# Kernel optimization log

Measured on AMD Instinct MI355X. Metric: run time of the kernel, lower is better.

The kernel has to match this reference:

```python
import jax, jax.numpy as jnp
import numpy as np

B, S, HID, H = 2, 2048, 1024, 16
D_HEAD = HID // H  # 64
EPS = 1e-5


def _gammas():
    lo, hi = np.log(1.0 / 512.0), np.log(1.0 / 32.0)
    return (1.0 - np.exp(np.linspace(lo, hi, H))).astype(np.float32)


def _decay_mask():
    # D[h, n, m] = gamma_h^(n-m) for n >= m else 0  (causal exponential decay)
    gam = jnp.asarray(_gammas())                      # [H]
    pos = jnp.arange(S, dtype=jnp.float32)
    diff = pos[:, None] - pos[None, :]                # [S, S]
    keep = diff >= 0
    logg = jnp.log(gam)[:, None, None]                # [H,1,1]
    safe = jnp.where(keep, diff, 0.0)[None]           # avoid inf for masked entries
    return jnp.where(keep[None], jnp.exp(safe * logg), 0.0)  # [H, S, S]


def setup_inputs() -> dict:
    key = jax.random.key(0)
    ks = jax.random.split(key, 10)
    rn = lambda k, shape, s=1.0: jax.random.normal(k, shape, dtype=jnp.float32) * s
    return {
        "x": rn(ks[0], (B, S, HID)),
        "wq": rn(ks[1], (H, D_HEAD, D_HEAD), 1.0 / np.sqrt(D_HEAD)),
        "bq": rn(ks[2], (H, D_HEAD), 0.02),
        "wk": rn(ks[3], (H, D_HEAD, D_HEAD), 1.0 / np.sqrt(D_HEAD)),
        "bk": rn(ks[4], (H, D_HEAD), 0.02),
        "wv": rn(ks[5], (H, D_HEAD, D_HEAD), 1.0 / np.sqrt(D_HEAD)),
        "theta": rn(ks[6], (H, D_HEAD), 1.0 / D_HEAD),
        "gn_weight": jnp.ones((HID,), jnp.float32),
        "gn_bias": jnp.zeros((HID,), jnp.float32),
        "weight1": rn(ks[7], (HID, HID), 1.0 / HID),
        "weight2": rn(ks[8], (HID, HID), 1.0 / HID),
    }


def reference(x, wq, bq, wk, bk, wv, theta, gn_weight, gn_bias, weight1, weight2):
    # Per-head retention (all heads vectorized; torch loops over heads).
    xh = x.reshape(B, S, H, D_HEAD)
    q = jnp.einsum('bshd,hde->bshe', xh, wq) + bq
    k = jnp.einsum('bshd,hde->bshe', xh, wk) + bk
    v = jnp.einsum('bshd,hde->bshe', xh, wv)
    # Complex rotary factors exp(i*n*theta) on q, conj on k -> real part of q k^H:
    ang = jnp.arange(S, dtype=jnp.float32)[:, None, None] * theta[None]  # [S,H,d]
    cs, sn = jnp.cos(ang), jnp.sin(ang)
    scores = (jnp.einsum('bshd,bthd->bhst', q * cs, k * cs)
              + jnp.einsum('bshd,bthd->bhst', q * sn, k * sn))  # Re(QK^H) [B,H,S,S]
    scores = scores * _decay_mask()[None]                        # decay mask
    ret = jnp.einsum('bhst,bthd->bshd', scores, v)               # [B,S,H,d]
    # GroupNorm with groups = n_heads over channels (per-head normalization).
    mean = jnp.mean(ret, axis=-1, keepdims=True)
    var = jnp.var(ret, axis=-1, keepdims=True)
    retn = (ret - mean) * jax.lax.rsqrt(var + EPS)
    retn = retn.reshape(B, S, HID) * gn_weight + gn_bias
    # Swish gate on x @ W1, residual add, project with W2.
    gate = x @ weight1
    out = gate * jax.nn.sigmoid(gate) + retn
    return out @ weight2
```

## Files before the change

### kernel.cpp

```cpp
#include <hip/hip_runtime.h>
#include <cstdint>
#include <cstddef>

#define B_ 2
#define S_ 2048
#define HID_ 1024
#define H_ 16
#define DH_ 64

typedef __attribute__((ext_vector_type(8))) short short8;
typedef __attribute__((ext_vector_type(8))) unsigned short ushort8;
typedef __attribute__((ext_vector_type(4))) unsigned short ushort4v;
typedef __attribute__((ext_vector_type(4))) float floatx4;
typedef __attribute__((ext_vector_type(4))) float float4v;

static __device__ __forceinline__ unsigned short f2bf(float f) {
  unsigned int u = __float_as_uint(f);
  u += 0x7fffu + ((u >> 16) & 1u);
  return (unsigned short)(u >> 16);
}
static __device__ __forceinline__ float bf2f(unsigned short h) {
  return __uint_as_float(((unsigned int)h) << 16);
}

__global__ __launch_bounds__(256) void convert_kernel(
    const float* __restrict__ x, const float* __restrict__ w1,
    const float* __restrict__ w2, unsigned short* __restrict__ x_bf,
    unsigned short* __restrict__ w1t, unsigned short* __restrict__ w2t_hi,
    unsigned short* __restrict__ w2t_lo) {
  const int NX = B_ * S_ * HID_;
  const int NW = HID_ * HID_;
  int idx = blockIdx.x * 256 + threadIdx.x;
  if (idx < NX) {
    x_bf[idx] = f2bf(x[idx]);
  } else if (idx < NX + NW) {
    int i = idx - NX;
    int n = i >> 10, k = i & 1023;
    w1t[i] = f2bf(w1[k * HID_ + n]);
  } else if (idx < NX + 2 * NW) {
    int i = idx - NX - NW;
    int n = i >> 10, k = i & 1023;
    float v = w2[k * HID_ + n];
    unsigned short h = f2bf(v);
    w2t_hi[i] = h;
    w2t_lo[i] = f2bf(v - bf2f(h));
  }
}

__global__ __launch_bounds__(256) void qkv_kernel(
    const float* __restrict__ x, const float* __restrict__ wq,
    const float* __restrict__ bq, const float* __restrict__ wk,
    const float* __restrict__ bk, const float* __restrict__ wv,
    const float* __restrict__ theta,
    unsigned short* __restrict__ q_h, unsigned short* __restrict__ q_l,
    unsigned short* __restrict__ k_h, unsigned short* __restrict__ k_l,
    unsigned short* __restrict__ v_th, unsigned short* __restrict__ v_tl,
    int b) {
  __shared__ __align__(16) float xs[64 * 68];
  __shared__ __align__(16) float wqs[64 * 68];
  __shared__ __align__(16) float wks[64 * 68];
  __shared__ __align__(16) float wvs[64 * 68];

  int tid = threadIdx.x;
  int st = blockIdx.x, h = blockIdx.y;
  int s0 = st * 64;

#pragma unroll
  for (int i = 0; i < 4; ++i) {
    int cid = tid + i * 256;
    int r = cid >> 4, c4 = (cid & 15) * 4;
    *reinterpret_cast<float4v*>(&xs[r * 68 + c4]) =
        *reinterpret_cast<const float4v*>(x + ((size_t)(b * S_ + s0 + r)) * HID_ + h * DH_ + c4);
  }
#pragma unroll
  for (int i = 0; i < 4; ++i) {
    int cid = tid + i * 256;
    int d = cid >> 4, c4 = (cid & 15) * 4;
    *reinterpret_cast<float4v*>(&wqs[d * 68 + c4]) =
        *reinterpret_cast<const float4v*>(wq + (size_t)(h * DH_ + d) * DH_ + c4);
    *reinterpret_cast<float4v*>(&wks[d * 68 + c4]) =
        *reinterpret_cast<const float4v*>(wk + (size_t)(h * DH_ + d) * DH_ + c4);
    *reinterpret_cast<float4v*>(&wvs[d * 68 + c4]) =
        *reinterpret_cast<const float4v*>(wv + (size_t)(h * DH_ + d) * DH_ + c4);
  }
  __syncthreads();

  int rg = tid >> 3;
  int cg = tid & 7;
  int r0 = rg * 2, c0 = cg * 8;

  float aq[2][8], ak[2][8], av[2][8];
#pragma unroll
  for (int i = 0; i < 2; ++i)
#pragma unroll
    for (int j = 0; j < 8; ++j) { aq[i][j] = 0.f; ak[i][j] = 0.f; av[i][j] = 0.f; }

  for (int d = 0; d < 64; ++d) {
    float x0 = xs[(r0 + 0) * 68 + d];
    float x1 = xs[(r0 + 1) * 68 + d];
#pragma unroll
    for (int j = 0; j < 8; ++j) {
      float wqv = wqs[d * 68 + c0 + j];
      float wkv = wks[d * 68 + c0 + j];
      float wvv = wvs[d * 68 + c0 + j];
      aq[0][j] += x0 * wqv; aq[1][j] += x1 * wqv;
      ak[0][j] += x0 * wkv; ak[1][j] += x1 * wkv;
      av[0][j] += x0 * wvv; av[1][j] += x1 * wvv;
    }
  }

  float thv[8], bqv[8], bkv[8];
#pragma unroll
  for (int j = 0; j < 8; ++j) {
    thv[j] = theta[h * DH_ + c0 + j];
    bqv[j] = bq[h * DH_ + c0 + j];
    bkv[j] = bk[h * DH_ + c0 + j];
  }

  __syncthreads();
  unsigned short* VtH = reinterpret_cast<unsigned short*>(xs);
  unsigned short* VtL = reinterpret_cast<unsigned short*>(wqs);

#pragma unroll
  for (int i = 0; i < 2; ++i) {
    int s = s0 + r0 + i;
    size_t qb = ((size_t)h * S_ + s) * 128;
    ushort8 qch, qcl, qsh, qsl, kch, kcl, ksh, ksl;
#pragma unroll
    for (int j = 0; j < 8; ++j) {
      float q = aq[i][j] + bqv[j];
      float k = ak[i][j] + bkv[j];
      float ang = (float)s * thv[j];
      float cs = cosf(ang), sn = sinf(ang);
      float qc = q * cs, qs = q * sn;
      unsigned short hq1 = f2bf(qc);
      qch[j] = hq1;
      qcl[j] = f2bf(qc - bf2f(hq1));
      unsigned short hq2 = f2bf(qs);
      qsh[j] = hq2;
      qsl[j] = f2bf(qs - bf2f(hq2));
      float kc = k * cs, ksn = k * sn;
      unsigned short h1 = f2bf(kc);
      kch[j] = h1;
      kcl[j] = f2bf(kc - bf2f(h1));
      unsigned short h2 = f2bf(ksn);
      ksh[j] = h2;
      ksl[j] = f2bf(ksn - bf2f(h2));
      float vv = av[i][j];
      unsigned short vh1 = f2bf(vv);
      VtH[(c0 + j) * 72 + (r0 + i)] = vh1;
      VtL[(c0 + j) * 72 + (r0 + i)] = f2bf(vv - bf2f(vh1));
    }
    *reinterpret_cast<ushort8*>(q_h + qb + c0) = qch;
    *reinterpret_cast<ushort8*>(q_h + qb + 64 + c0) = qsh;
    *reinterpret_cast<ushort8*>(q_l + qb + c0) = qcl;
    *reinterpret_cast<ushort8*>(q_l + qb + 64 + c0) = qsl;
    *reinterpret_cast<ushort8*>(k_h + qb + c0) = kch;
    *reinterpret_cast<ushort8*>(k_h + qb + 64 + c0) = ksh;
    *reinterpret_cast<ushort8*>(k_l + qb + c0) = kcl;
    *reinterpret_cast<ushort8*>(k_l + qb + 64 + c0) = ksl;
  }
  __syncthreads();
#pragma unroll
  for (int i = 0; i < 2; ++i) {
    int cid = tid + i * 256;
    int d = cid >> 3, t8 = (cid & 7) * 8;
    size_t gb = ((size_t)(h * 64 + d)) * S_ + s0 + t8;
    *reinterpret_cast<ushort8*>(v_th + gb) = *reinterpret_cast<const ushort8*>(&VtH[d * 72 + t8]);
    *reinterpret_cast<ushort8*>(v_tl + gb) = *reinterpret_cast<const ushort8*>(&VtL[d * 72 + t8]);
  }
}

#define SCOFF(row, colb)   ((row) * 256 + ((colb) ^ (((row) & 7) << 4)))

__global__ __launch_bounds__(256) void retention_split_kernel(
    const unsigned short* __restrict__ q_h, const unsigned short* __restrict__ q_l,
    const unsigned short* __restrict__ k_h, const unsigned short* __restrict__ k_l,
    const unsigned short* __restrict__ v_th, const unsigned short* __restrict__ v_tl,
    float* __restrict__ partial) {
  __shared__ __align__(16) unsigned short Kh[64 * 128];
  __shared__ __align__(16) unsigned short Kl[64 * 128];
  __shared__ __align__(16) unsigned short Vh[64 * 64];
  __shared__ __align__(16) unsigned short Vl[64 * 64];
  __shared__ __align__(16) float Sc[64 * 64];

  char* KhB = (char*)Kh;
  char* KlB = (char*)Kl;
  char* VhB = (char*)Vh;
  char* VlB = (char*)Vl;
  char* ScB = (char*)Sc;

  int tid = threadIdx.x;
  int w = tid >> 6;
  int lane = tid & 63, ln = lane & 15, quad = lane >> 4;
  int wr = w >> 1, wc = w & 1;
  int f = blockIdx.x;
  int h = ((f & 7) << 1) | ((f >> 3) & 1);
  int half = (f >> 4) & 1;
  int qt = 31 - (f >> 5);
  int s0 = qt * 64;

  int m = (qt + 2) >> 1;
  int kt0 = half ? m : 0;
  int kt1 = half ? (qt + 1) : m;

  const float lo_c = -6.2383246250395075f, hi_c = -3.4657359027997265f;
  float gam = 1.f - __expf(lo_c + (hi_c - lo_c) * ((float)h * (1.f / 15.f)));
  float logg = __logf(gam);

  float rowf[2][4], colf[2];
#pragma unroll
  for (int rt = 0; rt < 2; ++rt)
#pragma unroll
    for (int rr = 0; rr < 4; ++rr)
      rowf[rt][rr] = __expf((float)(wr * 32 + rt * 16 + quad * 4 + rr) * logg);
#pragma unroll
  for (int ns = 0; ns < 2; ++ns)
    colf[ns] = __expf(-(float)(wc * 32 + ns * 16 + ln) * logg);

  const unsigned short* khb = k_h + (size_t)h * S_ * 128;
  const unsigned short* klb = k_l + (size_t)h * S_ * 128;
  const unsigned short* vhb = v_th + (size_t)h * 64 * S_;
  const unsigned short* vlb = v_tl + (size_t)h * 64 * S_;

  short8 qfh[2][4], qfl[2][4];
#pragma unroll
  for (int rt = 0; rt < 2; ++rt) {
    int sQ = s0 + wr * 32 + rt * 16 + ln;
    const unsigned short* qhp = q_h + ((size_t)h * S_ + sQ) * 128 + quad * 8;
    const unsigned short* qlp = q_l + ((size_t)h * S_ + sQ) * 128 + quad * 8;
#pragma unroll
    for (int c = 0; c < 4; ++c) {
      qfh[rt][c] = *reinterpret_cast<const short8*>(qhp + c * 32);
      qfl[rt][c] = *reinterpret_cast<const short8*>(qlp + c * 32);
    }
  }

  floatx4 accO[4];
#pragma unroll
  for (int i = 0; i < 4; ++i) accO[i] = (floatx4){0.f, 0.f, 0.f, 0.f};

  ushort8 skh[4], skl[4], svh[2], svl[2];
  {
    int t00 = kt0 * 64;
#pragma unroll
    for (int i = 0; i < 4; ++i) {
      int cid = tid + i * 256;
      int r = cid >> 4, c8 = (cid & 15) * 8;
      skh[i] = *reinterpret_cast<const ushort8*>(khb + ((size_t)(t00 + r)) * 128 + c8);
      skl[i] = *reinterpret_cast<const ushort8*>(klb + ((size_t)(t00 + r)) * 128 + c8);
    }
#pragma unroll
    for (int i = 0; i < 2; ++i) {
      int cid = tid + i * 256;
      int d = cid >> 3, t8 = (cid & 7) * 8;
      svh[i] = *reinterpret_cast<const ushort8*>(vhb + (size_t)d * S_ + t00 + t8);
      svl[i] = *reinterpret_cast<const ushort8*>(vlb + (size_t)d * S_ + t00 + t8);
    }
#pragma unroll
    for (int i = 0; i < 4; ++i) {
      int cid = tid + i * 256;
      int r = cid >> 4;
      int ko = r * 256 + (((cid & 15) * 16) ^ ((r & 7) << 4));
      *reinterpret_cast<ushort8*>(KhB + ko) = skh[i];
      *reinterpret_cast<ushort8*>(KlB + ko) = skl[i];
    }
#pragma unroll
    for (int i = 0; i < 2; ++i) {
      int cid = tid + i * 256;
      int d = cid >> 3;
      int vo = d * 128 + (((cid & 7) * 16) ^ ((d & 7) << 4));
      *reinterpret_cast<ushort8*>(VhB + vo) = svh[i];
      *reinterpret_cast<ushort8*>(VlB + vo) = svl[i];
    }
    if (kt0 + 1 < kt1) {
      int t01 = (kt0 + 1) * 64;
#pragma unroll
      for (int i = 0; i < 4; ++i) {
        int cid = tid + i * 256;
        int r = cid >> 4, c8 = (cid & 15) * 8;
        skh[i] = *reinterpret_cast<const ushort8*>(khb + ((size_t)(t01 + r)) * 128 + c8);
        skl[i] = *reinterpret_cast<const ushort8*>(klb + ((size_t)(t01 + r)) * 128 + c8);
      }
#pragma unroll
      for (int i = 0; i < 2; ++i) {
        int cid = tid + i * 256;
        int d = cid >> 3, t8 = (cid & 7) * 8;
        svh[i] = *reinterpret_cast<const ushort8*>(vhb + (size_t)d * S_ + t01 + t8);
        svl[i] = *reinterpret_cast<const ushort8*>(vlb + (size_t)d * S_ + t01 + t8);
      }
    }
  }
  __syncthreads();

  for (int kt = kt0; kt < kt1; ++kt) {
    floatx4 accS[2][2];
#pragma unroll
    for (int rt = 0; rt < 2; ++rt)
#pragma unroll
      for (int ns = 0; ns < 2; ++ns) accS[rt][ns] = (floatx4){0.f, 0.f, 0.f, 0.f};
#pragma unroll
    for (int ns = 0; ns < 2; ++ns) {
      int krow = wc * 32 + ns * 16 + ln;
#pragma unroll
      for (int ks = 0; ks < 4; ++ks) {
        int off = krow * 256 + ((ks * 64 + quad * 16) ^ ((ln & 7) << 4));
        short8 kh = *reinterpret_cast<const short8*>(KhB + off);
        short8 kl = *reinterpret_cast<const short8*>(KlB + off);
#pragma unroll
        for (int rt = 0; rt < 2; ++rt) {
          accS[rt][ns] = __builtin_amdgcn_mfma_f32_16x16x32_bf16(qfh[rt][ks], kh, accS[rt][ns], 0, 0, 0);
          accS[rt][ns] = __builtin_amdgcn_mfma_f32_16x16x32_bf16(qfl[rt][ks], kh, accS[rt][ns], 0, 0, 0);
          accS[rt][ns] = __builtin_amdgcn_mfma_f32_16x16x32_bf16(qfh[rt][ks], kl, accS[rt][ns], 0, 0, 0);
        }
      }
    }

    float tf = __expf((float)(64 * (qt - kt)) * logg);
    float trf[2][4];
#pragma unroll
    for (int rt = 0; rt < 2; ++rt)
#pragma unroll
      for (int rr = 0; rr < 4; ++rr) trf[rt][rr] = tf * rowf[rt][rr];
    if (kt < qt) {
#pragma unroll
      for (int rt = 0; rt < 2; ++rt)
#pragma unroll
        for (int ns = 0; ns < 2; ++ns) {
          int col = wc * 32 + ns * 16 + ln;
#pragma unroll
          for (int rr = 0; rr < 4; ++rr) {
            int row = wr * 32 + rt * 16 + quad * 4 + rr;
            *reinterpret_cast<float*>(ScB + SCOFF(row, col * 4)) =
                accS[rt][ns][rr] * trf[rt][rr] * colf[ns];
          }
        }
    } else {
#pragma unroll
      for (int rt = 0; rt < 2; ++rt)
#pragma unroll
        for (int ns = 0; ns < 2; ++ns) {
          int col = wc * 32 + ns * 16 + ln;
#pragma unroll
          for (int rr = 0; rr < 4; ++rr) {
            int row = wr * 32 + rt * 16 + quad * 4 + rr;
            float v = accS[rt][ns][rr] * trf[rt][rr] * colf[ns];
            *reinterpret_cast<float*>(ScB + SCOFF(row, col * 4)) =
                (row >= col) ? v : 0.f;
          }
        }
    }
    __syncthreads();

#pragma unroll
    for (int ks = 0; ks < 2; ++ks) {
      int prw = w * 16 + ln;
      int cb = ks * 128 + quad * 32;
      float4v p0 = *reinterpret_cast<const float4v*>(ScB + SCOFF(prw, cb));
      float4v p1 = *reinterpret_cast<const float4v*>(ScB + SCOFF(prw, cb + 16));
      short8 ph, pl;
#pragma unroll
      for (int j = 0; j < 4; ++j) {
        unsigned short hh = f2bf(p0[j]);
        ph[j] = (short)hh;
        pl[j] = (short)f2bf(p0[j] - bf2f(hh));
        unsigned short hh2 = f2bf(p1[j]);
        ph[4 + j] = (short)hh2;
        pl[4 + j] = (short)f2bf(p1[j] - bf2f(hh2));
      }
#pragma unroll
      for (int ds = 0; ds < 4; ++ds) {
        int d = ds * 16 + ln;
        int voff = d * 128 + ((ks * 64 + quad * 16) ^ ((ln & 7) << 4));
        short8 vh = *reinterpret_cast<const short8*>(VhB + voff);
        short8 vl = *reinterpret_cast<const short8*>(VlB + voff);
        accO[ds] = __builtin_amdgcn_mfma_f32_16x16x32_bf16(ph, vh, accO[ds], 0, 0, 0);
        accO[ds] = __builtin_amdgcn_mfma_f32_16x16x32_bf16(pl, vh, accO[ds], 0, 0, 0);
        accO[ds] = __builtin_amdgcn_mfma_f32_16x16x32_bf16(ph, vl, accO[ds], 0, 0, 0);
      }
    }

    __syncthreads();
    if (kt + 1 < kt1) {
#pragma unroll
      for (int i = 0; i < 4; ++i) {
        int cid = tid + i * 256;
        int r = cid >> 4;
        int ko = r * 256 + (((cid & 15) * 16) ^ ((r & 7) << 4));
        *reinterpret_cast<ushort8*>(KhB + ko) = skh[i];
        *reinterpret_cast<ushort8*>(KlB + ko) = skl[i];
      }
#pragma unroll
      for (int i = 0; i < 2; ++i) {
        int cid = tid + i * 256;
        int d = cid >> 3;
        int vo = d * 128 + (((cid & 7) * 16) ^ ((d & 7) << 4));
        *reinterpret_cast<ushort8*>(VhB + vo) = svh[i];
        *reinterpret_cast<ushort8*>(VlB + vo) = svl[i];
      }
      if (kt + 2 < kt1) {
        int t0n = (kt + 2) * 64;
#pragma unroll
        for (int i = 0; i < 4; ++i) {
          int cid = tid + i * 256;
          int r = cid >> 4, c8 = (cid & 15) * 8;
          skh[i] = *reinterpret_cast<const ushort8*>(khb + ((size_t)(t0n + r)) * 128 + c8);
          skl[i] = *reinterpret_cast<const ushort8*>(klb + ((size_t)(t0n + r)) * 128 + c8);
        }
#pragma unroll
        for (int i = 0; i < 2; ++i) {
          int cid = tid + i * 256;
          int d = cid >> 3, t8 = (cid & 7) * 8;
          svh[i] = *reinterpret_cast<const ushort8*>(vhb + (size_t)d * S_ + t0n + t8);
          svl[i] = *reinterpret_cast<const ushort8*>(vlb + (size_t)d * S_ + t0n + t8);
        }
      }
      __syncthreads();
    }
  }

  float* pout = partial + ((size_t)(((h * 32 + qt) << 1) + half)) * 4096;
#pragma unroll
  for (int ds = 0; ds < 4; ++ds) {
#pragma unroll
    for (int rr = 0; rr < 4; ++rr) {
      pout[(w * 16 + quad * 4 + rr) * 64 + ds * 16 + ln] = accO[ds][rr];
    }
  }
}

__global__ __launch_bounds__(256) void combine_gn_kernel(
    const float* __restrict__ partial, const float* __restrict__ gn_w,
    const float* __restrict__ gn_b, float* __restrict__ retn, int b) {
  __shared__ float gnred[64][8];
  int tid = threadIdx.x;
  int qi = blockIdx.x;
  int h = qi >> 5, qt = qi & 31;
  const float* p0 = partial + (size_t)qi * 8192;
  const float* p1 = p0 + 4096;

  int r2 = tid >> 2;
  int sub = tid & 3;
  float a16[16];
#pragma unroll
  for (int c = 0; c < 4; ++c) {
    int o = r2 * 64 + sub * 16 + c * 4;
    float4v va = *reinterpret_cast<const float4v*>(p0 + o);
    float4v vb = *reinterpret_cast<const float4v*>(p1 + o);
#pragma unroll
    for (int j = 0; j < 4; ++j) a16[c * 4 + j] = va[j] + vb[j];
  }

  float psum = 0.f, psq = 0.f;
#pragma unroll
  for (int i = 0; i < 16; ++i) { psum += a16[i]; psq += a16[i] * a16[i]; }
  gnred[r2][sub] = psum;
  gnred[r2][4 + sub] = psq;
  float sum = gnred[r2][0] + gnred[r2][1] + gnred[r2][2] + gnred[r2][3];
  float sq = gnred[r2][4] + gnred[r2][5] + gnred[r2][6] + gnred[r2][7];
  float mean = sum * (1.f / 64.f);
  float var = sq * (1.f / 64.f) - mean * mean;
  float rstd = rsqrtf(var + 1e-5f);

  size_t obase = ((size_t)(b * S_ + qt * 64 + r2)) * HID_ + h * DH_ + sub * 16;
#pragma unroll
  for (int i = 0; i < 16; ++i) {
    float gw = gn_w[h * DH_ + sub * 16 + i];
    float gb = gn_b[h * DH_ + sub * 16 + i];
    retn[obase + i] = (a16[i] - mean) * rstd * gw + gb;
  }
}

__global__ __launch_bounds__(256) void gemm_gate_kernel(
    const unsigned short* __restrict__ A, const unsigned short* __restrict__ Bt,
    const float* __restrict__ retn, unsigned short* __restrict__ pre_hi,
    unsigned short* __restrict__ pre_lo) {
  const int K = HID_;
  __shared__ __align__(16) unsigned short Al[128 * 56];
  __shared__ __align__(16) unsigned short Bl[64 * 56];

  int tid = threadIdx.x;
  int lane = tid & 63, ln = lane & 15, quad = lane >> 4;
  int w = tid >> 6, wm = w >> 1, wn = w & 1;
  int m0 = blockIdx.y * 128, n0 = blockIdx.x * 64;

  floatx4 acc[4][2];
#pragma unroll
  for (int i = 0; i < 4; ++i)
#pragma unroll
    for (int j = 0; j < 2; ++j) acc[i][j] = (floatx4){0.f, 0.f, 0.f, 0.f};

  for (int k0 = 0; k0 < K; k0 += 32) {
    __syncthreads();
#pragma unroll
    for (int i = 0; i < 2; ++i) {
      int cid = tid + i * 256;
      int r = cid >> 2, c8 = (cid & 3) * 8;
      *reinterpret_cast<ushort8*>(&Al[r * 56 + c8]) =
          *reinterpret_cast<const ushort8*>(A + (size_t)(m0 + r) * K + k0 + c8);
    }
    {
      int r = tid >> 2, c8 = (tid & 3) * 8;
      *reinterpret_cast<ushort8*>(&Bl[r * 56 + c8]) =
          *reinterpret_cast<const ushort8*>(Bt + (size_t)(n0 + r) * K + k0 + c8);
    }
    __syncthreads();

    short8 af[4], bfr[2];
#pragma unroll
    for (int i = 0; i < 4; ++i)
      af[i] = *reinterpret_cast<const short8*>(&Al[(wm * 64 + i * 16 + ln) * 56 + quad * 8]);
#pragma unroll
    for (int i = 0; i < 2; ++i)
      bfr[i] = *reinterpret_cast<const short8*>(&Bl[(wn * 32 + i * 16 + ln) * 56 + quad * 8]);
#pragma unroll
    for (int mi = 0; mi < 4; ++mi)
#pragma unroll
      for (int ni = 0; ni < 2; ++ni)
        acc[mi][ni] = __builtin_amdgcn_mfma_f32_16x16x32_bf16(af[mi], bfr[ni], acc[mi][ni], 0, 0, 0);
  }

#pragma unroll
  for (int mi = 0; mi < 4; ++mi) {
#pragma unroll
    for (int r = 0; r < 4; ++r) {
      int row = m0 + wm * 64 + mi * 16 + quad * 4 + r;
#pragma unroll
      for (int ni = 0; ni < 2; ++ni) {
        int col = n0 + wn * 32 + ni * 16 + ln;
        float g = acc[mi][ni][r];
        float val = g * (1.f / (1.f + __expf(-g))) + retn[(size_t)row * HID_ + col];
        unsigned short hh = f2bf(val);
        size_t oidx = (size_t)row * HID_ + col;
        pre_hi[oidx] = hh;
        pre_lo[oidx] = f2bf(val - bf2f(hh));
      }
    }
  }
}

__global__ __launch_bounds__(256) void gemm_out_kernel(
    const unsigned short* __restrict__ Ah, const unsigned short* __restrict__ Alo,
    const unsigned short* __restrict__ Bth, const unsigned short* __restrict__ Btlo,
    float* __restrict__ out_f) {
  const int K = HID_;
  __shared__ __align__(16) unsigned short AhS[128 * 56];
  __shared__ __align__(16) unsigned short AlS[128 * 56];
  __shared__ __align__(16) unsigned short BhS[64 * 56];
  __shared__ __align__(16) unsigned short BlS[64 * 56];

  int tid = threadIdx.x;
  int lane = tid & 63, ln = lane & 15, quad = lane >> 4;
  int w = tid >> 6, wm = w >> 1, wn = w & 1;
  int m0 = blockIdx.y * 128, n0 = blockIdx.x * 64;

  floatx4 acc[4][2];
#pragma unroll
  for (int i = 0; i < 4; ++i)
#pragma unroll
    for (int j = 0; j < 2; ++j) acc[i][j] = (floatx4){0.f, 0.f, 0.f, 0.f};

  for (int k0 = 0; k0 < K; k0 += 32) {
    __syncthreads();
#pragma unroll
    for (int i = 0; i < 2; ++i) {
      int cid = tid + i * 256;
      int r = cid >> 2, c8 = (cid & 3) * 8;
      size_t ga = (size_t)(m0 + r) * K + k0 + c8;
      *reinterpret_cast<ushort8*>(&AhS[r * 56 + c8]) = *reinterpret_cast<const ushort8*>(Ah + ga);
      *reinterpret_cast<ushort8*>(&AlS[r * 56 + c8]) = *reinterpret_cast<const ushort8*>(Alo + ga);
    }
    {
      int r = tid >> 2, c8 = (tid & 3) * 8;
      size_t gb = (size_t)(n0 + r) * K + k0 + c8;
      *reinterpret_cast<ushort8*>(&BhS[r * 56 + c8]) = *reinterpret_cast<const ushort8*>(Bth + gb);
      *reinterpret_cast<ushort8*>(&BlS[r * 56 + c8]) = *reinterpret_cast<const ushort8*>(Btlo + gb);
    }
    __syncthreads();

    short8 afh[4], afl[4], bfh[2], bfl[2];
#pragma unroll
    for (int i = 0; i < 4; ++i) {
      int ao = (wm * 64 + i * 16 + ln) * 56 + quad * 8;
      afh[i] = *reinterpret_cast<const short8*>(&AhS[ao]);
      afl[i] = *reinterpret_cast<const short8*>(&AlS[ao]);
    }
#pragma unroll
    for (int i = 0; i < 2; ++i) {
      int bo = (wn * 32 + i * 16 + ln) * 56 + quad * 8;
      bfh[i] = *reinterpret_cast<const short8*>(&BhS[bo]);
      bfl[i] = *reinterpret_cast<const short8*>(&BlS[bo]);
    }
#pragma unroll
    for (int mi = 0; mi < 4; ++mi)
#pragma unroll
      for (int ni = 0; ni < 2; ++ni) {
        floatx4 a = acc[mi][ni];
        a = __builtin_amdgcn_mfma_f32_16x16x32_bf16(afh[mi], bfh[ni], a, 0, 0, 0);
        a = __builtin_amdgcn_mfma_f32_16x16x32_bf16(afl[mi], bfh[ni], a, 0, 0, 0);
        a = __builtin_amdgcn_mfma_f32_16x16x32_bf16(afh[mi], bfl[ni], a, 0, 0, 0);
        acc[mi][ni] = a;
      }
  }

#pragma unroll
  for (int mi = 0; mi < 4; ++mi) {
#pragma unroll
    for (int r = 0; r < 4; ++r) {
      int row = m0 + wm * 64 + mi * 16 + quad * 4 + r;
#pragma unroll
      for (int ni = 0; ni < 2; ++ni) {
        int col = n0 + wn * 32 + ni * 16 + ln;
        out_f[(size_t)row * HID_ + col] = acc[mi][ni][r];
      }
    }
  }
}

extern "C" void kernel_launch(void* const* d_in, const int* in_sizes, int n_in,
                              void* d_out, int out_size, void* d_ws,
                              size_t ws_size, hipStream_t stream) {
  (void)in_sizes; (void)n_in; (void)out_size; (void)ws_size;
  const float* x = (const float*)d_in[0];
  const float* wq = (const float*)d_in[1];
  const float* bq = (const float*)d_in[2];
  const float* wk = (const float*)d_in[3];
  const float* bk = (const float*)d_in[4];
  const float* wv = (const float*)d_in[5];
  const float* theta = (const float*)d_in[6];
  const float* gn_w = (const float*)d_in[7];
  const float* gn_b = (const float*)d_in[8];
  const float* w1 = (const float*)d_in[9];
  const float* w2 = (const float*)d_in[10];

  const size_t MB = 1024 * 1024;
  char* ws = (char*)d_ws;
  unsigned short* x_bf   = (unsigned short*)(ws + 0 * MB);
  unsigned short* w1t    = (unsigned short*)(ws + 8 * MB);
  unsigned short* w2t_hi = (unsigned short*)(ws + 10 * MB);
  unsigned short* w2t_lo = (unsigned short*)(ws + 12 * MB);
  unsigned short* q_h    = (unsigned short*)(ws + 14 * MB);
  unsigned short* q_l    = (unsigned short*)(ws + 22 * MB);
  unsigned short* k_h    = (unsigned short*)(ws + 30 * MB);
  unsigned short* k_l    = (unsigned short*)(ws + 38 * MB);
  unsigned short* v_th   = (unsigned short*)(ws + 46 * MB);
  unsigned short* v_tl   = (unsigned short*)(ws + 50 * MB);
  float*          retn   = (float*)(ws + 54 * MB);
  float*          partial= (float*)(ws + 70 * MB);
  unsigned short* pre_hi = (unsigned short*)(ws + 14 * MB);
  unsigned short* pre_lo = (unsigned short*)(ws + 22 * MB);
  float* out = (float*)d_out;

  convert_kernel<<<dim3(24576), 256, 0, stream>>>(x, w1, w2, x_bf, w1t, w2t_hi, w2t_lo);
  for (int b = 0; b < B_; ++b) {
    qkv_kernel<<<dim3(S_ / 64, H_), 256, 0, stream>>>(
        x, wq, bq, wk, bk, wv, theta, q_h, q_l, k_h, k_l, v_th, v_tl, b);
    retention_split_kernel<<<dim3(1024), 256, 0, stream>>>(
        q_h, q_l, k_h, k_l, v_th, v_tl, partial);
    combine_gn_kernel<<<dim3(512), 256, 0, stream>>>(
        partial, gn_w, gn_b, retn, b);
  }
  gemm_gate_kernel<<<dim3(HID_ / 64, (B_ * S_) / 128), 256, 0, stream>>>(
      x_bf, w1t, retn, pre_hi, pre_lo);
  gemm_out_kernel<<<dim3(HID_ / 64, (B_ * S_) / 128), 256, 0, stream>>>(
      pre_hi, pre_lo, w2t_hi, w2t_lo, out);
}
```

Measured before the change: 338.0 us.

## Double-buffer V in retention, add MFMA priority, shrink and prefetch GEMM tiles

The retention kernel now double-buffers the V tile in shared memory, so the next K/V tiles are stored between the score and PV phases, and one barrier per iteration is removed. The MFMA sections are wrapped in s_setprio to favour matrix issue. Both output GEMMs shrink their M tile from 128 to 64 rows, which doubles the grid, and they prefetch the next K-slice into registers before the barrier. A missing __syncthreads is also added in the GroupNorm reduction, which fixes a race at a small cost. The changes trade extra shared memory and less per-block reuse for more overlap and more blocks in flight.

Result: faster. 327.2 us (-3.2%).

```diff
diff --git a/kernel.cpp b/kernel.cpp
--- a/kernel.cpp
+++ b/kernel.cpp
@@ -180,8 +180,8 @@
     float* __restrict__ partial) {
   __shared__ __align__(16) unsigned short Kh[64 * 128];
   __shared__ __align__(16) unsigned short Kl[64 * 128];
-  __shared__ __align__(16) unsigned short Vh[64 * 64];
-  __shared__ __align__(16) unsigned short Vl[64 * 64];
+  __shared__ __align__(16) unsigned short Vh[2][64 * 64];
+  __shared__ __align__(16) unsigned short Vl[2][64 * 64];
   __shared__ __align__(16) float Sc[64 * 64];
 
   char* KhB = (char*)Kh;
@@ -294,11 +294,13 @@
   __syncthreads();
 
   for (int kt = kt0; kt < kt1; ++kt) {
+    int vb = (kt - kt0) & 1;
     floatx4 accS[2][2];
 #pragma unroll
     for (int rt = 0; rt < 2; ++rt)
 #pragma unroll
       for (int ns = 0; ns < 2; ++ns) accS[rt][ns] = (floatx4){0.f, 0.f, 0.f, 0.f};
+    __builtin_amdgcn_s_setprio(1);
 #pragma unroll
     for (int ns = 0; ns < 2; ++ns) {
       int krow = wc * 32 + ns * 16 + ln;
@@ -315,6 +317,7 @@
         }
       }
     }
+    __builtin_amdgcn_s_setprio(0);
 
     float tf = __expf((float)(64 * (qt - kt)) * logg);
     float trf[2][4];
@@ -352,6 +355,43 @@
     }
     __syncthreads();
 
+    if (kt + 1 < kt1) {
+#pragma unroll
+      for (int i = 0; i < 4; ++i) {
+        int cid = tid + i * 256;
+        int r = cid >> 4;
+        int ko = r * 256 + (((cid & 15) * 16) ^ ((r & 7) << 4));
+        *reinterpret_cast<ushort8*>(KhB + ko) = skh[i];
+        *reinterpret_cast<ushort8*>(KlB + ko) = skl[i];
+      }
+#pragma unroll
+      for (int i = 0; i < 2; ++i) {
+        int cid = tid + i * 256;
+        int d = cid >> 3;
+        int vo = (vb ^ 1) * 8192 + d * 128 + (((cid & 7) * 16) ^ ((d & 7) << 4));
+        *reinterpret_cast<ushort8*>(VhB + vo) = svh[i];
+        *reinterpret_cast<ushort8*>(VlB + vo) = svl[i];
+      }
+      if (kt + 2 < kt1) {
+        int t0n = (kt + 2) * 64;
+#pragma unroll
+        for (int i = 0; i < 4; ++i) {
+          int cid = tid + i * 256;
+          int r = cid >> 4, c8 = (cid & 15) * 8;
+          skh[i] = *reinterpret_cast<const ushort8*>(khb + ((size_t)(t0n + r)) * 128 + c8);
+          skl[i] = *reinterpret_cast<const ushort8*>(klb + ((size_t)(t0n + r)) * 128 + c8);
+        }
+#pragma unroll
+        for (int i = 0; i < 2; ++i) {
+          int cid = tid + i * 256;
+          int d = cid >> 3, t8 = (cid & 7) * 8;
+          svh[i] = *reinterpret_cast<const ushort8*>(vhb + (size_t)d * S_ + t0n + t8);
+          svl[i] = *reinterpret_cast<const ushort8*>(vlb + (size_t)d * S_ + t0n + t8);
+        }
+      }
+    }
+
+    __builtin_amdgcn_s_setprio(1);
 #pragma unroll
     for (int ks = 0; ks < 2; ++ks) {
       int prw = w * 16 + ln;
@@ -371,7 +411,7 @@
 #pragma unroll
       for (int ds = 0; ds < 4; ++ds) {
         int d = ds * 16 + ln;
-        int voff = d * 128 + ((ks * 64 + quad * 16) ^ ((ln & 7) << 4));
+        int voff = vb * 8192 + d * 128 + ((ks * 64 + quad * 16) ^ ((ln & 7) << 4));
         short8 vh = *reinterpret_cast<const short8*>(VhB + voff);
         short8 vl = *reinterpret_cast<const short8*>(VlB + voff);
         accO[ds] = __builtin_amdgcn_mfma_f32_16x16x32_bf16(ph, vh, accO[ds], 0, 0, 0);
@@ -379,44 +419,9 @@
         accO[ds] = __builtin_amdgcn_mfma_f32_16x16x32_bf16(ph, vl, accO[ds], 0, 0, 0);
       }
     }
+    __builtin_amdgcn_s_setprio(0);
 
     __syncthreads();
-    if (kt + 1 < kt1) {
-#pragma unroll
-      for (int i = 0; i < 4; ++i) {
-        int cid = tid + i * 256;
-        int r = cid >> 4;
-        int ko = r * 256 + (((cid & 15) * 16) ^ ((r & 7) << 4));
-        *reinterpret_cast<ushort8*>(KhB + ko) = skh[i];
-        *reinterpret_cast<ushort8*>(KlB + ko) = skl[i];
-      }
-#pragma unroll
-      for (int i = 0; i < 2; ++i) {
-        int cid = tid + i * 256;
-        int d = cid >> 3;
-        int vo = d * 128 + (((cid & 7) * 16) ^ ((d & 7) << 4));
-        *reinterpret_cast<ushort8*>(VhB + vo) = svh[i];
-        *reinterpret_cast<ushort8*>(VlB + vo) = svl[i];
-      }
-      if (kt + 2 < kt1) {
-        int t0n = (kt + 2) * 64;
-#pragma unroll
-        for (int i = 0; i < 4; ++i) {
-          int cid = tid + i * 256;
-          int r = cid >> 4, c8 = (cid & 15) * 8;
-          skh[i] = *reinterpret_cast<const ushort8*>(khb + ((size_t)(t0n + r)) * 128 + c8);
-          skl[i] = *reinterpret_cast<const ushort8*>(klb + ((size_t)(t0n + r)) * 128 + c8);
-        }
-#pragma unroll
-        for (int i = 0; i < 2; ++i) {
-          int cid = tid + i * 256;
-          int d = cid >> 3, t8 = (cid & 7) * 8;
-          svh[i] = *reinterpret_cast<const ushort8*>(vhb + (size_t)d * S_ + t0n + t8);
-          svl[i] = *reinterpret_cast<const ushort8*>(vlb + (size_t)d * S_ + t0n + t8);
-        }
-      }
-      __syncthreads();
-    }
   }
 
   float* pout = partial + ((size_t)(((h * 32 + qt) << 1) + half)) * 4096;
@@ -456,6 +461,7 @@
   for (int i = 0; i < 16; ++i) { psum += a16[i]; psq += a16[i] * a16[i]; }
   gnred[r2][sub] = psum;
   gnred[r2][4 + sub] = psq;
+  __syncthreads();
   float sum = gnred[r2][0] + gnred[r2][1] + gnred[r2][2] + gnred[r2][3];
   float sq = gnred[r2][4] + gnred[r2][5] + gnred[r2][6] + gnred[r2][7];
   float mean = sum * (1.f / 64.f);
@@ -476,55 +482,53 @@
     const float* __restrict__ retn, unsigned short* __restrict__ pre_hi,
     unsigned short* __restrict__ pre_lo) {
   const int K = HID_;
-  __shared__ __align__(16) unsigned short Al[128 * 56];
+  __shared__ __align__(16) unsigned short Al[64 * 56];
   __shared__ __align__(16) unsigned short Bl[64 * 56];
 
   int tid = threadIdx.x;
   int lane = tid & 63, ln = lane & 15, quad = lane >> 4;
   int w = tid >> 6, wm = w >> 1, wn = w & 1;
-  int m0 = blockIdx.y * 128, n0 = blockIdx.x * 64;
-
-  floatx4 acc[4][2];
-#pragma unroll
-  for (int i = 0; i < 4; ++i)
+  int m0 = blockIdx.y * 64, n0 = blockIdx.x * 64;
+
+  floatx4 acc[2][2];
+#pragma unroll
+  for (int i = 0; i < 2; ++i)
 #pragma unroll
     for (int j = 0; j < 2; ++j) acc[i][j] = (floatx4){0.f, 0.f, 0.f, 0.f};
 
+  int rr_ = tid >> 2, cc_ = (tid & 3) * 8;
+
+  ushort8 ra = *reinterpret_cast<const ushort8*>(A + (size_t)(m0 + rr_) * K + cc_);
+  ushort8 rb = *reinterpret_cast<const ushort8*>(Bt + (size_t)(n0 + rr_) * K + cc_);
+
   for (int k0 = 0; k0 < K; k0 += 32) {
+    *reinterpret_cast<ushort8*>(&Al[rr_ * 56 + cc_]) = ra;
+    *reinterpret_cast<ushort8*>(&Bl[rr_ * 56 + cc_]) = rb;
+    if (k0 + 32 < K) {
+      ra = *reinterpret_cast<const ushort8*>(A + (size_t)(m0 + rr_) * K + k0 + 32 + cc_);
+      rb = *reinterpret_cast<const ushort8*>(Bt + (size_t)(n0 + rr_) * K + k0 + 32 + cc_);
+    }
     __syncthreads();
+
+    short8 af[2], bfr[2];
 #pragma unroll
     for (int i = 0; i < 2; ++i) {
-      int cid = tid + i * 256;
-      int r = cid >> 2, c8 = (cid & 3) * 8;
-      *reinterpret_cast<ushort8*>(&Al[r * 56 + c8]) =
-          *reinterpret_cast<const ushort8*>(A + (size_t)(m0 + r) * K + k0 + c8);
-    }
-    {
-      int r = tid >> 2, c8 = (tid & 3) * 8;
-      *reinterpret_cast<ushort8*>(&Bl[r * 56 + c8]) =
-          *reinterpret_cast<const ushort8*>(Bt + (size_t)(n0 + r) * K + k0 + c8);
-    }
-    __syncthreads();
-
-    short8 af[4], bfr[2];
-#pragma unroll
-    for (int i = 0; i < 4; ++i)
-      af[i] = *reinterpret_cast<const short8*>(&Al[(wm * 64 + i * 16 + ln) * 56 + quad * 8]);
-#pragma unroll
-    for (int i = 0; i < 2; ++i)
+      af[i] = *reinterpret_cast<const short8*>(&Al[(wm * 32 + i * 16 + ln) * 56 + quad * 8]);
       bfr[i] = *reinterpret_cast<const short8*>(&Bl[(wn * 32 + i * 16 + ln) * 56 + quad * 8]);
-#pragma unroll
-    for (int mi = 0; mi < 4; ++mi)
+    }
+#pragma unroll
+    for (int mi = 0; mi < 2; ++mi)
 #pragma unroll
       for (int ni = 0; ni < 2; ++ni)
         acc[mi][ni] = __builtin_amdgcn_mfma_f32_16x16x32_bf16(af[mi], bfr[ni], acc[mi][ni], 0, 0, 0);
-  }
-
-#pragma unroll
-  for (int mi = 0; mi < 4; ++mi) {
+    __syncthreads();
+  }
+
+#pragma unroll
+  for (int mi = 0; mi < 2; ++mi) {
 #pragma unroll
     for (int r = 0; r < 4; ++r) {
-      int row = m0 + wm * 64 + mi * 16 + quad * 4 + r;
+      int row = m0 + wm * 32 + mi * 16 + quad * 4 + r;
 #pragma unroll
       for (int ni = 0; ni < 2; ++ni) {
         int col = n0 + wn * 32 + ni * 16 + ln;
@@ -544,55 +548,61 @@
     const unsigned short* __restrict__ Bth, const unsigned short* __restrict__ Btlo,
     float* __restrict__ out_f) {
   const int K = HID_;
-  __shared__ __align__(16) unsigned short AhS[128 * 56];
-  __shared__ __align__(16) unsigned short AlS[128 * 56];
+  __shared__ __align__(16) unsigned short AhS[64 * 56];
+  __shared__ __align__(16) unsigned short AlS[64 * 56];
   __shared__ __align__(16) unsigned short BhS[64 * 56];
   __shared__ __align__(16) unsigned short BlS[64 * 56];
 
   int tid = threadIdx.x;
   int lane = tid & 63, ln = lane & 15, quad = lane >> 4;
   int w = tid >> 6, wm = w >> 1, wn = w & 1;
-  int m0 = blockIdx.y * 128, n0 = blockIdx.x * 64;
-
-  floatx4 acc[4][2];
-#pragma unroll
-  for (int i = 0; i < 4; ++i)
+  int m0 = blockIdx.y * 64, n0 = blockIdx.x * 64;
+
+  floatx4 acc[2][2];
+#pragma unroll
+  for (int i = 0; i < 2; ++i)
 #pragma unroll
     for (int j = 0; j < 2; ++j) acc[i][j] = (floatx4){0.f, 0.f, 0.f, 0.f};
 
+  int rr_ = tid >> 2, cc_ = (tid & 3) * 8;
+
+  ushort8 rah, ral, rbh, rbl;
+  {
+    size_t ga = (size_t)(m0 + rr_) * K + cc_;
+    rah = *reinterpret_cast<const ushort8*>(Ah + ga);
+    ral = *reinterpret_cast<const ushort8*>(Alo + ga);
+    size_t gb = (size_t)(n0 + rr_) * K + cc_;
+    rbh = *reinterpret_cast<const ushort8*>(Bth + gb);
+    rbl = *reinterpret_cast<const ushort8*>(Btlo + gb);
+  }
+
   for (int k0 = 0; k0 < K; k0 += 32) {
+    *reinterpret_cast<ushort8*>(&AhS[rr_ * 56 + cc_]) = rah;
+    *reinterpret_cast<ushort8*>(&AlS[rr_ * 56 + cc_]) = ral;
+    *reinterpret_cast<ushort8*>(&BhS[rr_ * 56 + cc_]) = rbh;
+    *reinterpret_cast<ushort8*>(&BlS[rr_ * 56 + cc_]) = rbl;
+    if (k0 + 32 < K) {
+      size_t ga = (size_t)(m0 + rr_) * K + k0 + 32 + cc_;
+      rah = *reinterpret_cast<const ushort8*>(Ah + ga);
+      ral = *reinterpret_cast<const ushort8*>(Alo + ga);
+      size_t gb = (size_t)(n0 + rr_) * K + k0 + 32 + cc_;
+      rbh = *reinterpret_cast<const ushort8*>(Bth + gb);
+      rbl = *reinterpret_cast<const ushort8*>(Btlo + gb);
+    }
     __syncthreads();
+
+    short8 afh[2], afl[2], bfh[2], bfl[2];
 #pragma unroll
     for (int i = 0; i < 2; ++i) {
-      int cid = tid + i * 256;
-      int r = cid >> 2, c8 = (cid & 3) * 8;
-      size_t ga = (size_t)(m0 + r) * K + k0 + c8;
-      *reinterpret_cast<ushort8*>(&AhS[r * 56 + c8]) = *reinterpret_cast<const ushort8*>(Ah + ga);
-      *reinterpret_cast<ushort8*>(&AlS[r * 56 + c8]) = *reinterpret_cast<const ushort8*>(Alo + ga);
-    }
-    {
-      int r = tid >> 2, c8 = (tid & 3) * 8;
-      size_t gb = (size_t)(n0 + r) * K + k0 + c8;
-      *reinterpret_cast<ushort8*>(&BhS[r * 56 + c8]) = *reinterpret_cast<const ushort8*>(Bth + gb);
-      *reinterpret_cast<ushort8*>(&BlS[r * 56 + c8]) = *reinterpret_cast<const ushort8*>(Btlo + gb);
-    }
-    __syncthreads();
-
-    short8 afh[4], afl[4], bfh[2], bfl[2];
-#pragma unroll
-    for (int i = 0; i < 4; ++i) {
-      int ao = (wm * 64 + i * 16 + ln) * 56 + quad * 8;
+      int ao = (wm * 32 + i * 16 + ln) * 56 + quad * 8;
+      int bo = (wn * 32 + i * 16 + ln) * 56 + quad * 8;
       afh[i] = *reinterpret_cast<const short8*>(&AhS[ao]);
       afl[i] = *reinterpret_cast<const short8*>(&AlS[ao]);
-    }
-#pragma unroll
-    for (int i = 0; i < 2; ++i) {
-      int bo = (wn * 32 + i * 16 + ln) * 56 + quad * 8;
       bfh[i] = *reinterpret_cast<const short8*>(&BhS[bo]);
       bfl[i] = *reinterpret_cast<const short8*>(&BlS[bo]);
     }
 #pragma unroll
-    for (int mi = 0; mi < 4; ++mi)
+    for (int mi = 0; mi < 2; ++mi)
 #pragma unroll
       for (int ni = 0; ni < 2; ++ni) {
         floatx4 a = acc[mi][ni];
@@ -601,13 +611,14 @@
         a = __builtin_amdgcn_mfma_f32_16x16x32_bf16(afh[mi], bfl[ni], a, 0, 0, 0);
         acc[mi][ni] = a;
       }
-  }
-
-#pragma unroll
-  for (int mi = 0; mi < 4; ++mi) {
+    __syncthreads();
+  }
+
+#pragma unroll
+  for (int mi = 0; mi < 2; ++mi) {
 #pragma unroll
     for (int r = 0; r < 4; ++r) {
-      int row = m0 + wm * 64 + mi * 16 + quad * 4 + r;
+      int row = m0 + wm * 32 + mi * 16 + quad * 4 + r;
 #pragma unroll
       for (int ni = 0; ni < 2; ++ni) {
         int col = n0 + wn * 32 + ni * 16 + ln;
@@ -660,8 +671,8 @@
     combine_gn_kernel<<<dim3(512), 256, 0, stream>>>(
         partial, gn_w, gn_b, retn, b);
   }
-  gemm_gate_kernel<<<dim3(HID_ / 64, (B_ * S_) / 128), 256, 0, stream>>>(
+  gemm_gate_kernel<<<dim3(HID_ / 64, (B_ * S_) / 64), 256, 0, stream>>>(
       x_bf, w1t, retn, pre_hi, pre_lo);
-  gemm_out_kernel<<<dim3(HID_ / 64, (B_ * S_) / 128), 256, 0, stream>>>(
+  gemm_out_kernel<<<dim3(HID_ / 64, (B_ * S_) / 64), 256, 0, stream>>>(
       pre_hi, pre_lo, w2t_hi, w2t_lo, out);
 }
```
